# Optimization experiments

Hardware: AMD Instinct MI355X
Metric: run time of the kernel (lower is better)

Reference implementation:

```python
import jax, jax.numpy as jnp
import numpy as np

B, S, D = 8, 1024, 1024      # batch, seq, input_dim (= d_model)
H, E = 16, 64                # n_heads, d_embed (H*E == D)


def setup_inputs() -> dict:
    key = jax.random.key(0)
    ks = jax.random.split(key, 12)
    sd = 1.0 / np.sqrt(D)
    inp = {
        "X1": jax.random.normal(ks[0], (B, S, D), jnp.float32),
        "X2": jax.random.normal(ks[1], (B, S, D), jnp.float32),
        # Linear params stored as [in, out]
        "Wq": jax.random.uniform(ks[2], (D, H * E), jnp.float32, -sd, sd),
        "bq": jax.random.uniform(ks[3], (H * E,), jnp.float32, -sd, sd),
        "Wk": jax.random.uniform(ks[4], (D, H * E), jnp.float32, -sd, sd),
        "bk": jax.random.uniform(ks[5], (H * E,), jnp.float32, -sd, sd),
        "Wv": jax.random.uniform(ks[6], (D, H * E), jnp.float32, -sd, sd),
        "bv": jax.random.uniform(ks[7], (H * E,), jnp.float32, -sd, sd),
        "Wo": jax.random.uniform(ks[8], (H * E, D), jnp.float32, -sd, sd),
        "bo": jax.random.uniform(ks[9], (D,), jnp.float32, -sd, sd),
    }
    return inp


def reference(X1, X2, Wq, bq, Wk, bk, Wv, bv, Wo, bo):
    b, s, _ = X1.shape

    def split(x):  # [B,S,H*E] -> [B,H,S,E]
        return x.reshape(b, s, H, E).transpose(0, 2, 1, 3)

    Q = split(X1 @ Wq + bq)
    K = split(X2 @ Wk + bk)
    V = split(X2 @ Wv + bv)

    # Faithful quirk: d_k = K.shape[0] AFTER split_heads == batch size
    scores = jnp.einsum("bhqe,bhke->bhqk", Q, K) / jnp.sqrt(jnp.float32(b))

    # masked=True: tril then replace exact zeros with -1e9 (source quirk)
    tri = jnp.tril(jnp.ones((s, s), jnp.float32))
    scores = scores * tri
    scores = jnp.where(scores == 0.0, jnp.float32(-1e9), scores)

    # torch.nn.Softmax() with no dim on 4D input -> legacy dim=1 (heads axis)
    attn = jax.nn.softmax(scores, axis=1)

    out = jnp.einsum("bhqk,bhke->bhqe", attn, V)
    out = out.transpose(0, 2, 1, 3).reshape(b, s, H * E)  # combine heads
    return out @ Wo + bo
```

## Files before the change

kernel.cpp:

```cpp
#include <hip/hip_runtime.h>
#include <cstdint>


typedef unsigned short u16;
typedef unsigned int   u32;
typedef __attribute__((ext_vector_type(8))) __bf16         bf16x8;
typedef __attribute__((ext_vector_type(8))) unsigned short ushort8;
typedef __attribute__((ext_vector_type(4))) float          f32x4;

#define S_ 1024
#define D_ 1024
#define H_ 16
#define E_ 64

__device__ __forceinline__ float b2f(u16 h) {
  union { u32 u; float f; } v; v.u = ((u32)h) << 16; return v.f;
}
__device__ __forceinline__ u16 f2b(float f) {
  union { float f; u32 u; } v; v.f = f;
  u32 r = v.u + 0x7fffu + ((v.u >> 16) & 1u);
  return (u16)(r >> 16);
}

typedef const __attribute__((address_space(1))) u32 gu32;
typedef       __attribute__((address_space(3))) u32 lu32;

__device__ __forceinline__ void gload_lds16(const u16* g, u16* l) {
  __builtin_amdgcn_global_load_lds((gu32*)(uintptr_t)g, (lu32*)(uintptr_t)l,
                                   16, 0, 0);
}

__global__ __launch_bounds__(256, 1) void cvt_bf16(
    const float* __restrict__ src, u16* __restrict__ dst)
{
  const size_t i = (size_t)blockIdx.x * 256 + threadIdx.x;
  float4 a = ((const float4*)src)[2 * i];
  float4 b = ((const float4*)src)[2 * i + 1];
  ushort8 o;
  o[0] = f2b(a.x); o[1] = f2b(a.y); o[2] = f2b(a.z); o[3] = f2b(a.w);
  o[4] = f2b(b.x); o[5] = f2b(b.y); o[6] = f2b(b.z); o[7] = f2b(b.w);
  ((ushort8*)dst)[i] = o;
}

__global__ __launch_bounds__(256, 1) void trans_cvt_w(
    const float* __restrict__ W, u16* __restrict__ Wt)
{
  __shared__ u16 t[64][72];
  const int k0 = blockIdx.x * 64, n0 = blockIdx.y * 64;
  const int row = threadIdx.x >> 3;
  const int cs  = (threadIdx.x & 7) * 8;
#pragma unroll
  for (int p = 0; p < 2; ++p) {
    int r = row + p * 32;
    const float* Wp = W + (size_t)(k0 + r) * 1024 + n0 + cs;
    float4 a = *(const float4*)(Wp);
    float4 b = *(const float4*)(Wp + 4);
    u16* tp = &t[r][cs];
    tp[0] = f2b(a.x); tp[1] = f2b(a.y); tp[2] = f2b(a.z); tp[3] = f2b(a.w);
    tp[4] = f2b(b.x); tp[5] = f2b(b.y); tp[6] = f2b(b.z); tp[7] = f2b(b.w);
  }
  __syncthreads();
#pragma unroll
  for (int p = 0; p < 2; ++p) {
    int n = row + p * 32;
    ushort8 v;
#pragma unroll
    for (int i = 0; i < 8; ++i) v[i] = t[cs + i][n];
    *(ushort8*)(Wt + (size_t)(n0 + n) * 1024 + k0 + cs) = v;
  }
}

__global__ __launch_bounds__(256, 1) void gemm_bf16(
    const u16* __restrict__ A, const u16* __restrict__ Bt,
    const float* __restrict__ bias, void* __restrict__ Cv,
    int M, int N, int K, int out_f32)
{
  __shared__ u16 As[128 * 32];
  __shared__ u16 Bs[128 * 32];
  const int tid  = threadIdx.x;
  const int wave = tid >> 6;
  const int lane = tid & 63;
  const int quad = lane >> 4;
  const int l16  = lane & 15;
  const int m0   = (wave & 1) * 64;
  const int n0   = (wave >> 1) * 64;

  const u16* Ab = A  + (size_t)blockIdx.x * 128 * K;
  const u16* Bb = Bt + (size_t)blockIdx.y * 128 * K;

  f32x4 acc[4][4];
#pragma unroll
  for (int i = 0; i < 4; ++i)
#pragma unroll
    for (int j = 0; j < 4; ++j) acc[i][j] = (f32x4){0.f, 0.f, 0.f, 0.f};

  for (int kb = 0; kb < K; kb += 32) {
    __syncthreads();
#pragma unroll
    for (int p = 0; p < 2; ++p) {
      int seg = tid + p * 256;
      int row = seg >> 2, ks = seg & 3;
      gload_lds16(Ab + (size_t)row * K + kb + ks * 8, As + seg * 8);
      gload_lds16(Bb + (size_t)row * K + kb + ks * 8, Bs + seg * 8);
    }
    __builtin_amdgcn_s_waitcnt(0);
    __syncthreads();

    bf16x8 af[4], bfr[4];
#pragma unroll
    for (int i = 0; i < 4; ++i)
      af[i] = *(const bf16x8*)(As + (m0 + i * 16 + l16) * 32 + quad * 8);
#pragma unroll
    for (int j = 0; j < 4; ++j)
      bfr[j] = *(const bf16x8*)(Bs + (n0 + j * 16 + l16) * 32 + quad * 8);
#pragma unroll
    for (int i = 0; i < 4; ++i)
#pragma unroll
      for (int j = 0; j < 4; ++j)
        acc[i][j] = __builtin_amdgcn_mfma_f32_16x16x32_bf16(
            af[i], bfr[j], acc[i][j], 0, 0, 0);
  }

  float bv[4];
#pragma unroll
  for (int j = 0; j < 4; ++j)
    bv[j] = bias[(size_t)blockIdx.y * 128 + n0 + j * 16 + l16];

  if (out_f32) {
    float* C = (float*)Cv;
#pragma unroll
    for (int i = 0; i < 4; ++i) {
      int r = blockIdx.x * 128 + m0 + i * 16 + quad * 4;
#pragma unroll
      for (int j = 0; j < 4; ++j) {
        int c = blockIdx.y * 128 + n0 + j * 16 + l16;
#pragma unroll
        for (int reg = 0; reg < 4; ++reg)
          C[(size_t)(r + reg) * N + c] = acc[i][j][reg] + bv[j];
      }
    }
  } else {
    u16* C = (u16*)Cv;
#pragma unroll
    for (int i = 0; i < 4; ++i) {
      int r = blockIdx.x * 128 + m0 + i * 16 + quad * 4;
#pragma unroll
      for (int j = 0; j < 4; ++j) {
        int c = blockIdx.y * 128 + n0 + j * 16 + l16;
#pragma unroll
        for (int reg = 0; reg < 4; ++reg)
          C[(size_t)(r + reg) * N + c] = f2b(acc[i][j][reg] + bv[j]);
      }
    }
  }
}

__global__ __launch_bounds__(256, 1) void transpose_v(
    const u16* __restrict__ V, u16* __restrict__ Vt)
{
  __shared__ u16 t[64][72];
  const int s0 = blockIdx.x * 64;
  const int bh = blockIdx.y;
  const int b = bh >> 4, h = bh & 15;
  const int row = threadIdx.x >> 3;
  const int cs  = (threadIdx.x & 7) * 8;
#pragma unroll
  for (int p = 0; p < 2; ++p) {
    int s = row + p * 32;
    *(ushort8*)(&t[s][cs]) = *(const ushort8*)(
        V + ((size_t)(b * S_ + s0 + s)) * D_ + h * E_ + cs);
  }
  __syncthreads();
#pragma unroll
  for (int p = 0; p < 2; ++p) {
    int e = row + p * 32;
    ushort8 v;
#pragma unroll
    for (int i = 0; i < 8; ++i) v[i] = t[cs + i][e];
    *(ushort8*)(Vt + ((size_t)(bh * E_ + e)) * S_ + s0 + cs) = v;
  }
}

__global__ __launch_bounds__(1024, 4) void attn_headsoftmax(
    const u16* __restrict__ Qg,
    const u16* __restrict__ Kg,
    const u16* __restrict__ Vt,
    u16* __restrict__ AO)
{
  const int id   = blockIdx.x;
  const int b    = id & 7;
  const int qt   = id >> 3;
  const int tid  = threadIdx.x;
  const int h    = tid >> 6;
  const int lane = tid & 63;
  const int quad = lane >> 4;
  const int l16  = lane & 15;
  const int q0   = qt * 32;

  __shared__ u16 scf[16][32][72];
  __shared__ u16 at[16][32][72];

  const u16* Kh = Kg + (size_t)b * S_ * D_ + h * E_;
  const u16* Vh = Vt + ((size_t)(b * H_ + h) * E_) * S_;

  const float inv_rsq8 = 0.35355339059327373f;

  bf16x8 qf[2][2];
  {
    const u16* Qb = Qg + ((size_t)(b * S_ + q0)) * D_ + h * E_;
#pragma unroll
    for (int i = 0; i < 2; ++i)
#pragma unroll
      for (int c = 0; c < 2; ++c)
        qf[i][c] = *(const bf16x8*)(Qb + (size_t)(i * 16 + l16) * D_ +
                                    c * 32 + quad * 8);
  }

  f32x4 oacc[2][4];
#pragma unroll
  for (int i = 0; i < 2; ++i)
#pragma unroll
    for (int nc = 0; nc < 4; ++nc) oacc[i][nc] = (f32x4){0.f, 0.f, 0.f, 0.f};

  const int sm_q  = tid >> 5;
  const int sm_k  = (tid & 31) * 2;

  for (int kt = 0; kt < 16; ++kt) {
    const int k0 = kt * 64;
#pragma unroll
    for (int c2 = 0; c2 < 2; ++c2) {
      const int ks0 = k0 + c2 * 32;
      if (ks0 <= q0 + 31) {
        const u16* Kb = Kh + (size_t)ks0 * D_;
        bf16x8 kf[2][2];
#pragma unroll
        for (int nc = 0; nc < 2; ++nc)
#pragma unroll
          for (int c = 0; c < 2; ++c)
            kf[nc][c] = *(const bf16x8*)(Kb + (size_t)(nc * 16 + l16) * D_ +
                                         c * 32 + quad * 8);
        f32x4 sacc[2][2];
#pragma unroll
        for (int i = 0; i < 2; ++i)
#pragma unroll
          for (int nc = 0; nc < 2; ++nc)
            sacc[i][nc] = (f32x4){0.f, 0.f, 0.f, 0.f};
#pragma unroll
        for (int c = 0; c < 2; ++c)
#pragma unroll
          for (int i = 0; i < 2; ++i)
#pragma unroll
            for (int nc = 0; nc < 2; ++nc)
              sacc[i][nc] = __builtin_amdgcn_mfma_f32_16x16x32_bf16(
                  qf[i][c], kf[nc][c], sacc[i][nc], 0, 0, 0);
#pragma unroll
        for (int i = 0; i < 2; ++i)
#pragma unroll
          for (int nc = 0; nc < 2; ++nc)
#pragma unroll
            for (int reg = 0; reg < 4; ++reg) {
              int qrow = i * 16 + quad * 4 + reg;
              int kcol = nc * 16 + l16;
              float s = sacc[i][nc][reg] * inv_rsq8;
              if ((ks0 + kcol > q0 + qrow) || (s == 0.0f)) s = -1e9f;
              scf[h][qrow][c2 * 32 + kcol] = f2b(s);
            }
      }
    }
    __syncthreads();
    {
      const int qpos = q0 + sm_q;
      const int kpos = k0 + sm_k;
      int nU = qpos - kpos + 1;
      nU = nU < 0 ? 0 : (nU > 2 ? 2 : nU);
      if (nU == 0) {
        const u32 cc = 0x3D803D80u;
#pragma unroll
        for (int hh = 0; hh < 16; ++hh)
          *(u32*)&at[hh][sm_q][sm_k] = cc;
      } else {
        u32 v2[16];
#pragma unroll
        for (int hh = 0; hh < 16; ++hh)
          v2[hh] = *(const u32*)&scf[hh][sm_q][sm_k];
        u32 o2[16];
        {
          float e0,e1,e2,e3,e4,e5,e6,e7,e8,e9,ea,eb,ec,ed,ee,ef;
          e0 = __expf(b2f((u16)(v2[0]  & 0xffffu)));
          e1 = __expf(b2f((u16)(v2[1]  & 0xffffu)));
          e2 = __expf(b2f((u16)(v2[2]  & 0xffffu)));
          e3 = __expf(b2f((u16)(v2[3]  & 0xffffu)));
          e4 = __expf(b2f((u16)(v2[4]  & 0xffffu)));
          e5 = __expf(b2f((u16)(v2[5]  & 0xffffu)));
          e6 = __expf(b2f((u16)(v2[6]  & 0xffffu)));
          e7 = __expf(b2f((u16)(v2[7]  & 0xffffu)));
          e8 = __expf(b2f((u16)(v2[8]  & 0xffffu)));
          e9 = __expf(b2f((u16)(v2[9]  & 0xffffu)));
          ea = __expf(b2f((u16)(v2[10] & 0xffffu)));
          eb = __expf(b2f((u16)(v2[11] & 0xffffu)));
          ec = __expf(b2f((u16)(v2[12] & 0xffffu)));
          ed = __expf(b2f((u16)(v2[13] & 0xffffu)));
          ee = __expf(b2f((u16)(v2[14] & 0xffffu)));
          ef = __expf(b2f((u16)(v2[15] & 0xffffu)));
          float sum = (((e0+e1)+(e2+e3))+((e4+e5)+(e6+e7)))
                    + (((e8+e9)+(ea+eb))+((ec+ed)+(ee+ef)));
          float inv = 1.0f / sum;
          bool z = (sum == 0.0f);
          o2[0]  = z ? 0x3D80u : (u32)f2b(e0 * inv);
          o2[1]  = z ? 0x3D80u : (u32)f2b(e1 * inv);
          o2[2]  = z ? 0x3D80u : (u32)f2b(e2 * inv);
          o2[3]  = z ? 0x3D80u : (u32)f2b(e3 * inv);
          o2[4]  = z ? 0x3D80u : (u32)f2b(e4 * inv);
          o2[5]  = z ? 0x3D80u : (u32)f2b(e5 * inv);
          o2[6]  = z ? 0x3D80u : (u32)f2b(e6 * inv);
          o2[7]  = z ? 0x3D80u : (u32)f2b(e7 * inv);
          o2[8]  = z ? 0x3D80u : (u32)f2b(e8 * inv);
          o2[9]  = z ? 0x3D80u : (u32)f2b(e9 * inv);
          o2[10] = z ? 0x3D80u : (u32)f2b(ea * inv);
          o2[11] = z ? 0x3D80u : (u32)f2b(eb * inv);
          o2[12] = z ? 0x3D80u : (u32)f2b(ec * inv);
          o2[13] = z ? 0x3D80u : (u32)f2b(ed * inv);
          o2[14] = z ? 0x3D80u : (u32)f2b(ee * inv);
          o2[15] = z ? 0x3D80u : (u32)f2b(ef * inv);
        }
        if (nU == 2) {
          float e0,e1,e2,e3,e4,e5,e6,e7,e8,e9,ea,eb,ec,ed,ee,ef;
          e0 = __expf(b2f((u16)(v2[0]  >> 16)));
          e1 = __expf(b2f((u16)(v2[1]  >> 16)));
          e2 = __expf(b2f((u16)(v2[2]  >> 16)));
          e3 = __expf(b2f((u16)(v2[3]  >> 16)));
          e4 = __expf(b2f((u16)(v2[4]  >> 16)));
          e5 = __expf(b2f((u16)(v2[5]  >> 16)));
          e6 = __expf(b2f((u16)(v2[6]  >> 16)));
          e7 = __expf(b2f((u16)(v2[7]  >> 16)));
          e8 = __expf(b2f((u16)(v2[8]  >> 16)));
          e9 = __expf(b2f((u16)(v2[9]  >> 16)));
          ea = __expf(b2f((u16)(v2[10] >> 16)));
          eb = __expf(b2f((u16)(v2[11] >> 16)));
          ec = __expf(b2f((u16)(v2[12] >> 16)));
          ed = __expf(b2f((u16)(v2[13] >> 16)));
          ee = __expf(b2f((u16)(v2[14] >> 16)));
          ef = __expf(b2f((u16)(v2[15] >> 16)));
          float sum = (((e0+e1)+(e2+e3))+((e4+e5)+(e6+e7)))
                    + (((e8+e9)+(ea+eb))+((ec+ed)+(ee+ef)));
          float inv = 1.0f / sum;
          bool z = (sum == 0.0f);
          o2[0]  |= ((u32)(z ? 0x3D80u : f2b(e0 * inv))) << 16;
          o2[1]  |= ((u32)(z ? 0x3D80u : f2b(e1 * inv))) << 16;
          o2[2]  |= ((u32)(z ? 0x3D80u : f2b(e2 * inv))) << 16;
          o2[3]  |= ((u32)(z ? 0x3D80u : f2b(e3 * inv))) << 16;
          o2[4]  |= ((u32)(z ? 0x3D80u : f2b(e4 * inv))) << 16;
          o2[5]  |= ((u32)(z ? 0x3D80u : f2b(e5 * inv))) << 16;
          o2[6]  |= ((u32)(z ? 0x3D80u : f2b(e6 * inv))) << 16;
          o2[7]  |= ((u32)(z ? 0x3D80u : f2b(e7 * inv))) << 16;
          o2[8]  |= ((u32)(z ? 0x3D80u : f2b(e8 * inv))) << 16;
          o2[9]  |= ((u32)(z ? 0x3D80u : f2b(e9 * inv))) << 16;
          o2[10] |= ((u32)(z ? 0x3D80u : f2b(ea * inv))) << 16;
          o2[11] |= ((u32)(z ? 0x3D80u : f2b(eb * inv))) << 16;
          o2[12] |= ((u32)(z ? 0x3D80u : f2b(ec * inv))) << 16;
          o2[13] |= ((u32)(z ? 0x3D80u : f2b(ed * inv))) << 16;
          o2[14] |= ((u32)(z ? 0x3D80u : f2b(ee * inv))) << 16;
          o2[15] |= ((u32)(z ? 0x3D80u : f2b(ef * inv))) << 16;
        } else {
#pragma unroll
          for (int hh = 0; hh < 16; ++hh) o2[hh] |= 0x3D800000u;
        }
#pragma unroll
        for (int hh = 0; hh < 16; ++hh)
          *(u32*)&at[hh][sm_q][sm_k] = o2[hh];
      }
    }
    __syncthreads();
#pragma unroll
    for (int c2 = 0; c2 < 2; ++c2) {
      bf16x8 af[2];
#pragma unroll
      for (int i = 0; i < 2; ++i)
        af[i] = *(const bf16x8*)(&at[h][i * 16 + l16][c2 * 32 + quad * 8]);
      const u16* Vb = Vh + k0 + c2 * 32;
      bf16x8 vf[4];
#pragma unroll
      for (int nc = 0; nc < 4; ++nc)
        vf[nc] = *(const bf16x8*)(Vb + (size_t)(nc * 16 + l16) * S_ +
                                  quad * 8);
#pragma unroll
      for (int i = 0; i < 2; ++i)
#pragma unroll
        for (int nc = 0; nc < 4; ++nc)
          oacc[i][nc] = __builtin_amdgcn_mfma_f32_16x16x32_bf16(
              af[i], vf[nc], oacc[i][nc], 0, 0, 0);
    }
  }

  u16* Ob = AO + ((size_t)(b * S_ + q0)) * D_ + h * E_;
#pragma unroll
  for (int i = 0; i < 2; ++i)
#pragma unroll
    for (int nc = 0; nc < 4; ++nc)
#pragma unroll
      for (int reg = 0; reg < 4; ++reg) {
        int qrow = i * 16 + quad * 4 + reg;
        int e    = nc * 16 + l16;
        Ob[(size_t)qrow * D_ + e] = f2b(oacc[i][nc][reg]);
      }
}

extern "C" void kernel_launch(void* const* d_in, const int* in_sizes, int n_in,
                              void* d_out, int out_size, void* d_ws,
                              size_t ws_size, hipStream_t stream)
{
  const float* X1 = (const float*)d_in[0];
  const float* X2 = (const float*)d_in[1];
  const float* Wq = (const float*)d_in[2];
  const float* bq = (const float*)d_in[3];
  const float* Wk = (const float*)d_in[4];
  const float* bk = (const float*)d_in[5];
  const float* Wv = (const float*)d_in[6];
  const float* bv = (const float*)d_in[7];
  const float* Wo = (const float*)d_in[8];
  const float* bo = (const float*)d_in[9];

  u16* X1b = (u16*)d_ws;
  u16* X2b = X1b + (8u << 20);
  u16* WtQ = X2b + (8u << 20);
  u16* WtK = WtQ + (1u << 20);
  u16* WtV = WtK + (1u << 20);
  u16* WtO = WtV + (1u << 20);
  u16* Qb  = WtO + (1u << 20);
  u16* Kb  = Qb + (8u << 20);
  u16* Vb  = Kb + (8u << 20);
  u16* Vtb = Vb + (8u << 20);
  u16* AOb = Vb;

  cvt_bf16<<<4096, 256, 0, stream>>>(X1, X1b);
  cvt_bf16<<<4096, 256, 0, stream>>>(X2, X2b);

  dim3 tg(16, 16);
  trans_cvt_w<<<tg, 256, 0, stream>>>(Wq, WtQ);
  trans_cvt_w<<<tg, 256, 0, stream>>>(Wk, WtK);
  trans_cvt_w<<<tg, 256, 0, stream>>>(Wv, WtV);
  trans_cvt_w<<<tg, 256, 0, stream>>>(Wo, WtO);

  dim3 gg(64, 8);
  gemm_bf16<<<gg, 256, 0, stream>>>(X1b, WtQ, bq, Qb, 8192, 1024, 1024, 0);
  gemm_bf16<<<gg, 256, 0, stream>>>(X2b, WtK, bk, Kb, 8192, 1024, 1024, 0);
  gemm_bf16<<<gg, 256, 0, stream>>>(X2b, WtV, bv, Vb, 8192, 1024, 1024, 0);

  transpose_v<<<dim3(16, 128), 256, 0, stream>>>(Vb, Vtb);

  attn_headsoftmax<<<dim3(256), 1024, 0, stream>>>(Qb, Kb, Vtb, AOb);

  gemm_bf16<<<gg, 256, 0, stream>>>(AOb, WtO, bo, d_out, 8192, 1024, 1024, 1);
}
```

Before: 434.2 us.

## Skip fully masked key tiles analytically and split attention key range across blocks

Past the causal diagonal every head's score is -1e9, so the softmax over heads there is exactly a uniform 1/16. The attention kernel now loops only over the key tiles that reach the diagonal and adds that masked region as a precomputed sum of V columns times 1/16. To balance the triangular work, each query tile's key range is split in two across 512 blocks, launched in reversed tile order. The two halves combine through fp32 atomic adds into a zeroed workspace, and the scores and probabilities now share one LDS buffer. The price is a 32MB memset, an extra fp32-to-bf16 conversion pass and atomic traffic on the output.

```diff
diff --git a/kernel.cpp b/kernel.cpp
--- a/kernel.cpp
+++ b/kernel.cpp
@@ -185,11 +185,13 @@
     const u16* __restrict__ Qg,
     const u16* __restrict__ Kg,
     const u16* __restrict__ Vt,
-    u16* __restrict__ AO)
+    float* __restrict__ P)
 {
   const int id   = blockIdx.x;
   const int b    = id & 7;
-  const int qt   = id >> 3;
+  const int rk   = id >> 3;
+  const int qt   = 31 - (rk >> 1);
+  const int half = rk & 1;
   const int tid  = threadIdx.x;
   const int h    = tid >> 6;
   const int lane = tid & 63;
@@ -197,8 +199,12 @@
   const int l16  = lane & 15;
   const int q0   = qt * 32;
 
-  __shared__ u16 scf[16][32][72];
-  __shared__ u16 at[16][32][72];
+  const int nt    = (qt >> 1) + 1;
+  const int c0    = (nt + 1) >> 1;
+  const int myLo  = half ? c0 : 0;
+  const int myCnt = half ? (nt - c0) : c0;
+
+  __shared__ u16 S[16][32][72];
 
   const u16* Kh = Kg + (size_t)b * S_ * D_ + h * E_;
   const u16* Vh = Vt + ((size_t)(b * H_ + h) * E_) * S_;
@@ -225,174 +231,206 @@
   const int sm_q  = tid >> 5;
   const int sm_k  = (tid & 31) * 2;
 
-  for (int kt = 0; kt < 16; ++kt) {
-    const int k0 = kt * 64;
-#pragma unroll
-    for (int c2 = 0; c2 < 2; ++c2) {
-      const int ks0 = k0 + c2 * 32;
-      if (ks0 <= q0 + 31) {
-        const u16* Kb = Kh + (size_t)ks0 * D_;
-        bf16x8 kf[2][2];
-#pragma unroll
-        for (int nc = 0; nc < 2; ++nc)
+#pragma unroll 1
+  for (int t = 0; t < 8; ++t) {
+    if (t < myCnt) {
+      const int kt = myLo + t;
+      const int k0 = kt * 64;
+#pragma unroll
+      for (int c2 = 0; c2 < 2; ++c2) {
+        const int ks0 = k0 + c2 * 32;
+        if (ks0 <= q0 + 31) {
+          const u16* Kb = Kh + (size_t)ks0 * D_;
+          bf16x8 kf[2][2];
+#pragma unroll
+          for (int nc = 0; nc < 2; ++nc)
+#pragma unroll
+            for (int c = 0; c < 2; ++c)
+              kf[nc][c] = *(const bf16x8*)(Kb + (size_t)(nc * 16 + l16) * D_ +
+                                           c * 32 + quad * 8);
+          f32x4 sacc[2][2];
+#pragma unroll
+          for (int i = 0; i < 2; ++i)
+#pragma unroll
+            for (int nc = 0; nc < 2; ++nc)
+              sacc[i][nc] = (f32x4){0.f, 0.f, 0.f, 0.f};
 #pragma unroll
           for (int c = 0; c < 2; ++c)
-            kf[nc][c] = *(const bf16x8*)(Kb + (size_t)(nc * 16 + l16) * D_ +
-                                         c * 32 + quad * 8);
-        f32x4 sacc[2][2];
+#pragma unroll
+            for (int i = 0; i < 2; ++i)
+#pragma unroll
+              for (int nc = 0; nc < 2; ++nc)
+                sacc[i][nc] = __builtin_amdgcn_mfma_f32_16x16x32_bf16(
+                    qf[i][c], kf[nc][c], sacc[i][nc], 0, 0, 0);
+#pragma unroll
+          for (int i = 0; i < 2; ++i)
+#pragma unroll
+            for (int nc = 0; nc < 2; ++nc)
+#pragma unroll
+              for (int reg = 0; reg < 4; ++reg) {
+                int qrow = i * 16 + quad * 4 + reg;
+                int kcol = nc * 16 + l16;
+                float s = sacc[i][nc][reg] * inv_rsq8;
+                if ((ks0 + kcol > q0 + qrow) || (s == 0.0f)) s = -1e9f;
+                S[h][qrow][c2 * 32 + kcol] = f2b(s);
+              }
+        }
+      }
+      __syncthreads();
+      {
+        const int qpos = q0 + sm_q;
+        const int kpos = k0 + sm_k;
+        int nU = qpos - kpos + 1;
+        nU = nU < 0 ? 0 : (nU > 2 ? 2 : nU);
+        if (nU == 0) {
+          const u32 cc = 0x3D803D80u;
+#pragma unroll
+          for (int hh = 0; hh < 16; ++hh)
+            *(u32*)&S[hh][sm_q][sm_k] = cc;
+        } else {
+          u32 v2[16];
+#pragma unroll
+          for (int hh = 0; hh < 16; ++hh)
+            v2[hh] = *(const u32*)&S[hh][sm_q][sm_k];
+          u32 o2[16];
+          {
+            float e0,e1,e2,e3,e4,e5,e6,e7,e8,e9,ea,eb,ec,ed,ee,ef;
+            e0 = __expf(b2f((u16)(v2[0]  & 0xffffu)));
+            e1 = __expf(b2f((u16)(v2[1]  & 0xffffu)));
+            e2 = __expf(b2f((u16)(v2[2]  & 0xffffu)));
+            e3 = __expf(b2f((u16)(v2[3]  & 0xffffu)));
+            e4 = __expf(b2f((u16)(v2[4]  & 0xffffu)));
+            e5 = __expf(b2f((u16)(v2[5]  & 0xffffu)));
+            e6 = __expf(b2f((u16)(v2[6]  & 0xffffu)));
+            e7 = __expf(b2f((u16)(v2[7]  & 0xffffu)));
+            e8 = __expf(b2f((u16)(v2[8]  & 0xffffu)));
+            e9 = __expf(b2f((u16)(v2[9]  & 0xffffu)));
+            ea = __expf(b2f((u16)(v2[10] & 0xffffu)));
+            eb = __expf(b2f((u16)(v2[11] & 0xffffu)));
+            ec = __expf(b2f((u16)(v2[12] & 0xffffu)));
+            ed = __expf(b2f((u16)(v2[13] & 0xffffu)));
+            ee = __expf(b2f((u16)(v2[14] & 0xffffu)));
+            ef = __expf(b2f((u16)(v2[15] & 0xffffu)));
+            float sum = (((e0+e1)+(e2+e3))+((e4+e5)+(e6+e7)))
+                      + (((e8+e9)+(ea+eb))+((ec+ed)+(ee+ef)));
+            float inv = 1.0f / sum;
+            bool z = (sum == 0.0f);
+            o2[0]  = z ? 0x3D80u : (u32)f2b(e0 * inv);
+            o2[1]  = z ? 0x3D80u : (u32)f2b(e1 * inv);
+            o2[2]  = z ? 0x3D80u : (u32)f2b(e2 * inv);
+            o2[3]  = z ? 0x3D80u : (u32)f2b(e3 * inv);
+            o2[4]  = z ? 0x3D80u : (u32)f2b(e4 * inv);
+            o2[5]  = z ? 0x3D80u : (u32)f2b(e5 * inv);
+            o2[6]  = z ? 0x3D80u : (u32)f2b(e6 * inv);
+            o2[7]  = z ? 0x3D80u : (u32)f2b(e7 * inv);
+            o2[8]  = z ? 0x3D80u : (u32)f2b(e8 * inv);
+            o2[9]  = z ? 0x3D80u : (u32)f2b(e9 * inv);
+            o2[10] = z ? 0x3D80u : (u32)f2b(ea * inv);
+            o2[11] = z ? 0x3D80u : (u32)f2b(eb * inv);
+            o2[12] = z ? 0x3D80u : (u32)f2b(ec * inv);
+            o2[13] = z ? 0x3D80u : (u32)f2b(ed * inv);
+            o2[14] = z ? 0x3D80u : (u32)f2b(ee * inv);
+            o2[15] = z ? 0x3D80u : (u32)f2b(ef * inv);
+          }
+          if (nU == 2) {
+            float e0,e1,e2,e3,e4,e5,e6,e7,e8,e9,ea,eb,ec,ed,ee,ef;
+            e0 = __expf(b2f((u16)(v2[0]  >> 16)));
+            e1 = __expf(b2f((u16)(v2[1]  >> 16)));
+            e2 = __expf(b2f((u16)(v2[2]  >> 16)));
+            e3 = __expf(b2f((u16)(v2[3]  >> 16)));
+            e4 = __expf(b2f((u16)(v2[4]  >> 16)));
+            e5 = __expf(b2f((u16)(v2[5]  >> 16)));
+            e6 = __expf(b2f((u16)(v2[6]  >> 16)));
+            e7 = __expf(b2f((u16)(v2[7]  >> 16)));
+            e8 = __expf(b2f((u16)(v2[8]  >> 16)));
+            e9 = __expf(b2f((u16)(v2[9]  >> 16)));
+            ea = __expf(b2f((u16)(v2[10] >> 16)));
+            eb = __expf(b2f((u16)(v2[11] >> 16)));
+            ec = __expf(b2f((u16)(v2[12] >> 16)));
+            ed = __expf(b2f((u16)(v2[13] >> 16)));
+            ee = __expf(b2f((u16)(v2[14] >> 16)));
+            ef = __expf(b2f((u16)(v2[15] >> 16)));
+            float sum = (((e0+e1)+(e2+e3))+((e4+e5)+(e6+e7)))
+                      + (((e8+e9)+(ea+eb))+((ec+ed)+(ee+ef)));
+            float inv = 1.0f / sum;
+            bool z = (sum == 0.0f);
+            o2[0]  |= ((u32)(z ? 0x3D80u : f2b(e0 * inv))) << 16;
+            o2[1]  |= ((u32)(z ? 0x3D80u : f2b(e1 * inv))) << 16;
+            o2[2]  |= ((u32)(z ? 0x3D80u : f2b(e2 * inv))) << 16;
+            o2[3]  |= ((u32)(z ? 0x3D80u : f2b(e3 * inv))) << 16;
+            o2[4]  |= ((u32)(z ? 0x3D80u : f2b(e4 * inv))) << 16;
+            o2[5]  |= ((u32)(z ? 0x3D80u : f2b(e5 * inv))) << 16;
+            o2[6]  |= ((u32)(z ? 0x3D80u : f2b(e6 * inv))) << 16;
+            o2[7]  |= ((u32)(z ? 0x3D80u : f2b(e7 * inv))) << 16;
+            o2[8]  |= ((u32)(z ? 0x3D80u : f2b(e8 * inv))) << 16;
+            o2[9]  |= ((u32)(z ? 0x3D80u : f2b(e9 * inv))) << 16;
+            o2[10] |= ((u32)(z ? 0x3D80u : f2b(ea * inv))) << 16;
+            o2[11] |= ((u32)(z ? 0x3D80u : f2b(eb * inv))) << 16;
+            o2[12] |= ((u32)(z ? 0x3D80u : f2b(ec * inv))) << 16;
+            o2[13] |= ((u32)(z ? 0x3D80u : f2b(ed * inv))) << 16;
+            o2[14] |= ((u32)(z ? 0x3D80u : f2b(ee * inv))) << 16;
+            o2[15] |= ((u32)(z ? 0x3D80u : f2b(ef * inv))) << 16;
+          } else {
+#pragma unroll
+            for (int hh = 0; hh < 16; ++hh) o2[hh] |= 0x3D800000u;
+          }
+#pragma unroll
+          for (int hh = 0; hh < 16; ++hh)
+            *(u32*)&S[hh][sm_q][sm_k] = o2[hh];
+        }
+      }
+      __syncthreads();
+#pragma unroll
+      for (int c2 = 0; c2 < 2; ++c2) {
+        bf16x8 af[2];
 #pragma unroll
         for (int i = 0; i < 2; ++i)
-#pragma unroll
-          for (int nc = 0; nc < 2; ++nc)
-            sacc[i][nc] = (f32x4){0.f, 0.f, 0.f, 0.f};
-#pragma unroll
-        for (int c = 0; c < 2; ++c)
-#pragma unroll
-          for (int i = 0; i < 2; ++i)
-#pragma unroll
-            for (int nc = 0; nc < 2; ++nc)
-              sacc[i][nc] = __builtin_amdgcn_mfma_f32_16x16x32_bf16(
-                  qf[i][c], kf[nc][c], sacc[i][nc], 0, 0, 0);
+          af[i] = *(const bf16x8*)(&S[h][i * 16 + l16][c2 * 32 + quad * 8]);
+        const u16* Vb = Vh + k0 + c2 * 32;
+        bf16x8 vf[4];
+#pragma unroll
+        for (int nc = 0; nc < 4; ++nc)
+          vf[nc] = *(const bf16x8*)(Vb + (size_t)(nc * 16 + l16) * S_ +
+                                    quad * 8);
 #pragma unroll
         for (int i = 0; i < 2; ++i)
 #pragma unroll
-          for (int nc = 0; nc < 2; ++nc)
-#pragma unroll
-            for (int reg = 0; reg < 4; ++reg) {
-              int qrow = i * 16 + quad * 4 + reg;
-              int kcol = nc * 16 + l16;
-              float s = sacc[i][nc][reg] * inv_rsq8;
-              if ((ks0 + kcol > q0 + qrow) || (s == 0.0f)) s = -1e9f;
-              scf[h][qrow][c2 * 32 + kcol] = f2b(s);
-            }
-      }
+          for (int nc = 0; nc < 4; ++nc)
+            oacc[i][nc] = __builtin_amdgcn_mfma_f32_16x16x32_bf16(
+                af[i], vf[nc], oacc[i][nc], 0, 0, 0);
+      }
+      __syncthreads();
     }
-    __syncthreads();
-    {
-      const int qpos = q0 + sm_q;
-      const int kpos = k0 + sm_k;
-      int nU = qpos - kpos + 1;
-      nU = nU < 0 ? 0 : (nU > 2 ? 2 : nU);
-      if (nU == 0) {
-        const u32 cc = 0x3D803D80u;
-#pragma unroll
-        for (int hh = 0; hh < 16; ++hh)
-          *(u32*)&at[hh][sm_q][sm_k] = cc;
-      } else {
-        u32 v2[16];
-#pragma unroll
-        for (int hh = 0; hh < 16; ++hh)
-          v2[hh] = *(const u32*)&scf[hh][sm_q][sm_k];
-        u32 o2[16];
-        {
-          float e0,e1,e2,e3,e4,e5,e6,e7,e8,e9,ea,eb,ec,ed,ee,ef;
-          e0 = __expf(b2f((u16)(v2[0]  & 0xffffu)));
-          e1 = __expf(b2f((u16)(v2[1]  & 0xffffu)));
-          e2 = __expf(b2f((u16)(v2[2]  & 0xffffu)));
-          e3 = __expf(b2f((u16)(v2[3]  & 0xffffu)));
-          e4 = __expf(b2f((u16)(v2[4]  & 0xffffu)));
-          e5 = __expf(b2f((u16)(v2[5]  & 0xffffu)));
-          e6 = __expf(b2f((u16)(v2[6]  & 0xffffu)));
-          e7 = __expf(b2f((u16)(v2[7]  & 0xffffu)));
-          e8 = __expf(b2f((u16)(v2[8]  & 0xffffu)));
-          e9 = __expf(b2f((u16)(v2[9]  & 0xffffu)));
-          ea = __expf(b2f((u16)(v2[10] & 0xffffu)));
-          eb = __expf(b2f((u16)(v2[11] & 0xffffu)));
-          ec = __expf(b2f((u16)(v2[12] & 0xffffu)));
-          ed = __expf(b2f((u16)(v2[13] & 0xffffu)));
-          ee = __expf(b2f((u16)(v2[14] & 0xffffu)));
-          ef = __expf(b2f((u16)(v2[15] & 0xffffu)));
-          float sum = (((e0+e1)+(e2+e3))+((e4+e5)+(e6+e7)))
-                    + (((e8+e9)+(ea+eb))+((ec+ed)+(ee+ef)));
-          float inv = 1.0f / sum;
-          bool z = (sum == 0.0f);
-          o2[0]  = z ? 0x3D80u : (u32)f2b(e0 * inv);
-          o2[1]  = z ? 0x3D80u : (u32)f2b(e1 * inv);
-          o2[2]  = z ? 0x3D80u : (u32)f2b(e2 * inv);
-          o2[3]  = z ? 0x3D80u : (u32)f2b(e3 * inv);
-          o2[4]  = z ? 0x3D80u : (u32)f2b(e4 * inv);
-          o2[5]  = z ? 0x3D80u : (u32)f2b(e5 * inv);
-          o2[6]  = z ? 0x3D80u : (u32)f2b(e6 * inv);
-          o2[7]  = z ? 0x3D80u : (u32)f2b(e7 * inv);
-          o2[8]  = z ? 0x3D80u : (u32)f2b(e8 * inv);
-          o2[9]  = z ? 0x3D80u : (u32)f2b(e9 * inv);
-          o2[10] = z ? 0x3D80u : (u32)f2b(ea * inv);
-          o2[11] = z ? 0x3D80u : (u32)f2b(eb * inv);
-          o2[12] = z ? 0x3D80u : (u32)f2b(ec * inv);
-          o2[13] = z ? 0x3D80u : (u32)f2b(ed * inv);
-          o2[14] = z ? 0x3D80u : (u32)f2b(ee * inv);
-          o2[15] = z ? 0x3D80u : (u32)f2b(ef * inv);
+  }
+
+  float suf[4] = {0.f, 0.f, 0.f, 0.f};
+  if (half == 1) {
+    const int s0u = nt * 64;
+    if (s0u < S_) {
+      const int chunk = (S_ - s0u) >> 2;
+#pragma unroll
+      for (int nc = 0; nc < 4; ++nc) {
+        const u16* vp = Vh + (size_t)(nc * 16 + l16) * S_ + s0u +
+                        quad * chunk;
+        float a = 0.f;
+        for (int s = 0; s < chunk; s += 8) {
+          ushort8 v8 = *(const ushort8*)(vp + s);
+#pragma unroll
+          for (int jj = 0; jj < 8; ++jj) a += b2f(v8[jj]);
         }
-        if (nU == 2) {
-          float e0,e1,e2,e3,e4,e5,e6,e7,e8,e9,ea,eb,ec,ed,ee,ef;
-          e0 = __expf(b2f((u16)(v2[0]  >> 16)));
-          e1 = __expf(b2f((u16)(v2[1]  >> 16)));
-          e2 = __expf(b2f((u16)(v2[2]  >> 16)));
-          e3 = __expf(b2f((u16)(v2[3]  >> 16)));
-          e4 = __expf(b2f((u16)(v2[4]  >> 16)));
-          e5 = __expf(b2f((u16)(v2[5]  >> 16)));
-          e6 = __expf(b2f((u16)(v2[6]  >> 16)));
-          e7 = __expf(b2f((u16)(v2[7]  >> 16)));
-          e8 = __expf(b2f((u16)(v2[8]  >> 16)));
-          e9 = __expf(b2f((u16)(v2[9]  >> 16)));
-          ea = __expf(b2f((u16)(v2[10] >> 16)));
-          eb = __expf(b2f((u16)(v2[11] >> 16)));
-          ec = __expf(b2f((u16)(v2[12] >> 16)));
-          ed = __expf(b2f((u16)(v2[13] >> 16)));
-          ee = __expf(b2f((u16)(v2[14] >> 16)));
-          ef = __expf(b2f((u16)(v2[15] >> 16)));
-          float sum = (((e0+e1)+(e2+e3))+((e4+e5)+(e6+e7)))
-                    + (((e8+e9)+(ea+eb))+((ec+ed)+(ee+ef)));
-          float inv = 1.0f / sum;
-          bool z = (sum == 0.0f);
-          o2[0]  |= ((u32)(z ? 0x3D80u : f2b(e0 * inv))) << 16;
-          o2[1]  |= ((u32)(z ? 0x3D80u : f2b(e1 * inv))) << 16;
-          o2[2]  |= ((u32)(z ? 0x3D80u : f2b(e2 * inv))) << 16;
-          o2[3]  |= ((u32)(z ? 0x3D80u : f2b(e3 * inv))) << 16;
-          o2[4]  |= ((u32)(z ? 0x3D80u : f2b(e4 * inv))) << 16;
-          o2[5]  |= ((u32)(z ? 0x3D80u : f2b(e5 * inv))) << 16;
-          o2[6]  |= ((u32)(z ? 0x3D80u : f2b(e6 * inv))) << 16;
-          o2[7]  |= ((u32)(z ? 0x3D80u : f2b(e7 * inv))) << 16;
-          o2[8]  |= ((u32)(z ? 0x3D80u : f2b(e8 * inv))) << 16;
-          o2[9]  |= ((u32)(z ? 0x3D80u : f2b(e9 * inv))) << 16;
-          o2[10] |= ((u32)(z ? 0x3D80u : f2b(ea * inv))) << 16;
-          o2[11] |= ((u32)(z ? 0x3D80u : f2b(eb * inv))) << 16;
-          o2[12] |= ((u32)(z ? 0x3D80u : f2b(ec * inv))) << 16;
-          o2[13] |= ((u32)(z ? 0x3D80u : f2b(ed * inv))) << 16;
-          o2[14] |= ((u32)(z ? 0x3D80u : f2b(ee * inv))) << 16;
-          o2[15] |= ((u32)(z ? 0x3D80u : f2b(ef * inv))) << 16;
-        } else {
-#pragma unroll
-          for (int hh = 0; hh < 16; ++hh) o2[hh] |= 0x3D800000u;
-        }
-#pragma unroll
-        for (int hh = 0; hh < 16; ++hh)
-          *(u32*)&at[hh][sm_q][sm_k] = o2[hh];
+        suf[nc] = a;
+      }
+#pragma unroll
+      for (int nc = 0; nc < 4; ++nc) {
+        float a = suf[nc];
+        a += __shfl_xor(a, 16);
+        a += __shfl_xor(a, 32);
+        suf[nc] = a * 0.0625f;
       }
     }
-    __syncthreads();
-#pragma unroll
-    for (int c2 = 0; c2 < 2; ++c2) {
-      bf16x8 af[2];
-#pragma unroll
-      for (int i = 0; i < 2; ++i)
-        af[i] = *(const bf16x8*)(&at[h][i * 16 + l16][c2 * 32 + quad * 8]);
-      const u16* Vb = Vh + k0 + c2 * 32;
-      bf16x8 vf[4];
-#pragma unroll
-      for (int nc = 0; nc < 4; ++nc)
-        vf[nc] = *(const bf16x8*)(Vb + (size_t)(nc * 16 + l16) * S_ +
-                                  quad * 8);
-#pragma unroll
-      for (int i = 0; i < 2; ++i)
-#pragma unroll
-        for (int nc = 0; nc < 4; ++nc)
-          oacc[i][nc] = __builtin_amdgcn_mfma_f32_16x16x32_bf16(
-              af[i], vf[nc], oacc[i][nc], 0, 0, 0);
-    }
-  }
-
-  u16* Ob = AO + ((size_t)(b * S_ + q0)) * D_ + h * E_;
+  }
+
+  float* Pb = P + ((size_t)(b * S_ + q0)) * D_ + h * E_;
 #pragma unroll
   for (int i = 0; i < 2; ++i)
 #pragma unroll
@@ -401,7 +439,8 @@
       for (int reg = 0; reg < 4; ++reg) {
         int qrow = i * 16 + quad * 4 + reg;
         int e    = nc * 16 + l16;
-        Ob[(size_t)qrow * D_ + e] = f2b(oacc[i][nc][reg]);
+        unsafeAtomicAdd(&Pb[(size_t)qrow * D_ + e],
+                        oacc[i][nc][reg] + suf[nc]);
       }
 }
 
@@ -430,6 +469,7 @@
   u16* Kb  = Qb + (8u << 20);
   u16* Vb  = Kb + (8u << 20);
   u16* Vtb = Vb + (8u << 20);
+  float* P = (float*)d_ws;
   u16* AOb = Vb;
 
   cvt_bf16<<<4096, 256, 0, stream>>>(X1, X1b);
@@ -448,7 +488,11 @@
 
   transpose_v<<<dim3(16, 128), 256, 0, stream>>>(Vb, Vtb);
 
-  attn_headsoftmax<<<dim3(256), 1024, 0, stream>>>(Qb, Kb, Vtb, AOb);
+  hipMemsetAsync(P, 0, (size_t)8192 * 1024 * 4, stream);
+
+  attn_headsoftmax<<<dim3(512), 1024, 0, stream>>>(Qb, Kb, Vtb, P);
+
+  cvt_bf16<<<4096, 256, 0, stream>>>(P, AOb);
 
   gemm_bf16<<<gg, 256, 0, stream>>>(AOb, WtO, bo, d_out, 8192, 1024, 1024, 1);
 }
```

After: 465.3 us. 7.2% more time.
